# Kernel tuning notes

Hardware: AMD Instinct MI355X
Metric: run time of the kernel (lower is better)

## Reference

```python
import jax, jax.numpy as jnp
import numpy as np

M = 0.4
EPS = 1e-3
S = 64.0


def setup_inputs() -> dict:
    key = jax.random.key(0)
    k1, k2, k3, k4 = jax.random.split(key, 4)
    B, C = 1024, 100000
    # cosine logits strictly inside (-1, 1) so acos is finite
    logits = jax.random.uniform(k1, (B, C), jnp.float32, minval=-0.99, maxval=0.99)
    # feature norms around the typical face-embedding range
    norms = jax.random.uniform(k2, (B, 1), jnp.float32, minval=5.0, maxval=35.0)
    labels = jax.random.randint(k3, (B,), 0, C, dtype=jnp.int64)
    neg = jax.random.uniform(k4, (B,)) < 0.05
    labels = jnp.where(neg, jnp.int64(-1), labels)
    return {"logits": logits, "norms": norms, "labels": labels}


def reference(logits, norms, labels):
    B, C = logits.shape
    pos = labels != -1                                   # [B]
    # safe_norms is detached in the original (clone().detach())
    sn = jax.lax.stop_gradient(jnp.clip(norms, 1e-3, 100.0))[:, 0]  # [B]
    posf = pos.astype(sn.dtype)
    cnt = jnp.sum(posf)
    mean = jnp.sum(sn * posf) / cnt                      # mean over positive rows
    var = jnp.sum(jnp.where(pos, (sn - mean) ** 2, 0.0)) / (cnt - 1.0)  # unbiased, like torch.std
    std = jnp.sqrt(var)
    margin_scaler = (sn - mean) / (std + EPS)            # [B]
    g_angular = -M * margin_scaler                        # added to theta at target column
    g_add = M + M * margin_scaler                         # subtracted from cos at target column

    rows = jnp.arange(B)
    theta = jnp.arccos(logits)                           # [B, C]
    # inject angular margin only at (row, label); 0 for skipped rows (label=-1 wraps harmlessly)
    theta = theta.at[rows, labels].add(jnp.where(pos, g_angular, 0.0))
    tl = jnp.cos(jnp.clip(theta, EPS, jnp.pi - EPS))     # [B, C]
    tl = tl.at[rows, labels].add(-jnp.where(pos, g_add, 0.0))
    # rows with label == -1 keep their original logits
    out = jnp.where(pos[:, None], tl, logits) * S
    return out
```

## Files before the change

kernel.cpp:

```cpp
#include <hip/hip_runtime.h>
#include <math.h>

#define MARGIN 0.4f
#define EPSF   1e-3f
#define SCALE  64.0f
#define ELEMS_PER_THREAD 16

typedef float vfloat4 __attribute__((ext_vector_type(4)));

__global__ __launch_bounds__(256)
void adaface_scale_kernel(const vfloat4* __restrict__ in,
                          vfloat4* __restrict__ out,
                          long n4, const float* __restrict__ in_s,
                          float* __restrict__ out_s, long n_tail_start, long n) {
    long nthreads = (long)gridDim.x * blockDim.x;
    long i = (long)blockIdx.x * blockDim.x + threadIdx.x;

#pragma unroll
    for (int j = 0; j < ELEMS_PER_THREAD; ++j) {
        long k = i + (long)j * nthreads;
        if (k < n4) {
            vfloat4 v = __builtin_nontemporal_load(&in[k]);
            v *= SCALE;
            __builtin_nontemporal_store(v, &out[k]);
        }
    }
    for (long k = n_tail_start + i; k < n; k += nthreads) {
        out_s[k] = in_s[k] * SCALE;
    }
}

__global__ __launch_bounds__(1024)
void adaface_fixup_kernel(const float* __restrict__ logits,
                          const float* __restrict__ norms,
                          const int* __restrict__ labels,
                          float* __restrict__ out, int B, int C) {
    __shared__ float red_a[16];
    __shared__ float red_b[16];
    __shared__ float s_cnt, s_mean, s_std;

    int tid  = threadIdx.x;
    int lane = tid & 63;
    int wave = tid >> 6;
    int nw   = (blockDim.x + 63) >> 6;

    float sn  = 0.0f;
    int   lab = -1;
    bool  pos = false;
    if (tid < B) {
        sn  = fminf(fmaxf(norms[tid], 1e-3f), 100.0f);
        lab = labels[tid];
        pos = (lab != -1);
    }

    float a = pos ? 1.0f : 0.0f;
    float b = pos ? sn : 0.0f;
    for (int off = 32; off >= 1; off >>= 1) {
        a += __shfl_down(a, off);
        b += __shfl_down(b, off);
    }
    if (lane == 0) { red_a[wave] = a; red_b[wave] = b; }
    __syncthreads();
    if (wave == 0) {
        float aa = (lane < nw) ? red_a[lane] : 0.0f;
        float bb = (lane < nw) ? red_b[lane] : 0.0f;
        for (int off = 32; off >= 1; off >>= 1) {
            aa += __shfl_down(aa, off);
            bb += __shfl_down(bb, off);
        }
        if (lane == 0) { s_cnt = aa; s_mean = bb / aa; }
    }
    __syncthreads();

    float mean = s_mean;
    float d = sn - mean;
    float v = pos ? d * d : 0.0f;
    for (int off = 32; off >= 1; off >>= 1) v += __shfl_down(v, off);
    if (lane == 0) red_a[wave] = v;
    __syncthreads();
    if (wave == 0) {
        float vv = (lane < nw) ? red_a[lane] : 0.0f;
        for (int off = 32; off >= 1; off >>= 1) vv += __shfl_down(vv, off);
        if (lane == 0) s_std = sqrtf(vv / (s_cnt - 1.0f));
    }
    __syncthreads();

    if (tid < B && pos) {
        float ms    = (sn - mean) / (s_std + EPSF);
        float g_ang = -MARGIN * ms;
        float g_add = MARGIN + MARGIN * ms;
        long idx = (long)tid * C + lab;
        float x = logits[idx];
        float theta = acosf(x) + g_ang;
        theta = fminf(fmaxf(theta, EPSF), (float)M_PI - EPSF);
        out[idx] = (cosf(theta) - g_add) * SCALE;
    }
}

extern "C" void kernel_launch(void* const* d_in, const int* in_sizes, int n_in,
                              void* d_out, int out_size, void* d_ws, size_t ws_size,
                              hipStream_t stream) {
    const float* logits = (const float*)d_in[0];
    const float* norms  = (const float*)d_in[1];
    const int*   labels = (const int*)d_in[2];
    float* out = (float*)d_out;

    int B = in_sizes[2];
    long n = (long)in_sizes[0];
    int C = (int)(n / B);

    long n4 = n / 4;
    long tail_start = n4 * 4;

    int block = 256;
    long grid_l = (n4 + (long)block * ELEMS_PER_THREAD - 1) / ((long)block * ELEMS_PER_THREAD);
    int grid = (int)grid_l;

    adaface_scale_kernel<<<grid, block, 0, stream>>>(
        (const vfloat4*)logits, (vfloat4*)out, n4,
        logits, out, tail_start, n);

    adaface_fixup_kernel<<<1, 1024, 0, stream>>>(logits, norms, labels, out, B, C);
}
```

Baseline: 147.9 us.

## Fuse margin fixup into streaming scale kernel with per-block target patching

Merges the separate single-block fixup kernel into the main scale kernel. Each block now owns a contiguous chunk and checks whether one of its at most two overlapping rows has its target column inside that chunk. Blocks that do recompute the norm mean and std redundantly, apply the angular margin, and patch the value into the vector store. This removes a second launch and its serial tail, at the cost of redundant reductions in target-holding blocks and a fixed limit of 1024 rows for the statistics.

Result: slower. 157.6 us (+6.5%).

```diff
diff --git a/kernel.cpp b/kernel.cpp
--- a/kernel.cpp
+++ b/kernel.cpp
@@ -4,96 +4,135 @@
 #define MARGIN 0.4f
 #define EPSF   1e-3f
 #define SCALE  64.0f
-#define ELEMS_PER_THREAD 16
+#define EPT    16
+#define BLK    256
 
 typedef float vfloat4 __attribute__((ext_vector_type(4)));
 
-__global__ __launch_bounds__(256)
-void adaface_scale_kernel(const vfloat4* __restrict__ in,
-                          vfloat4* __restrict__ out,
-                          long n4, const float* __restrict__ in_s,
-                          float* __restrict__ out_s, long n_tail_start, long n) {
-    long nthreads = (long)gridDim.x * blockDim.x;
-    long i = (long)blockIdx.x * blockDim.x + threadIdx.x;
+__global__ __launch_bounds__(BLK)
+void adaface_fused_kernel(const float* __restrict__ in_s,
+                          const float* __restrict__ norms,
+                          const int* __restrict__ labels,
+                          float* __restrict__ out_s,
+                          long n4, long n, int B, int C) {
+    const vfloat4* __restrict__ in  = (const vfloat4*)in_s;
+    vfloat4* __restrict__ out = (vfloat4*)out_s;
 
+    int  tid    = threadIdx.x;
+    long f4base = (long)blockIdx.x * (BLK * EPT);
+    long fstart = f4base * 4;
+    long fend   = fstart + (long)BLK * EPT * 4;
+
+    int  row0     = (int)(fstart / C);
+    long rowsplit = (long)(row0 + 1) * C;
+    int  r1       = row0 + 1;
+
+    int  lab0 = (row0 < B) ? labels[row0] : -1;
+    int  lab1 = (r1   < B) ? labels[r1]   : -1;
+    long t0 = (lab0 != -1) ? (long)row0 * C + lab0 : (long)-1;
+    long t1 = (lab1 != -1) ? (long)r1   * C + lab1 : (long)-1;
+    bool has0 = (t0 >= fstart) && (t0 < fend);
+    bool has1 = (t1 >= fstart) && (t1 < fend);
+    bool full = (f4base + (long)BLK * EPT) <= n4;
+
+    if (full && !(has0 || has1)) {
 #pragma unroll
-    for (int j = 0; j < ELEMS_PER_THREAD; ++j) {
-        long k = i + (long)j * nthreads;
-        if (k < n4) {
+        for (int j = 0; j < EPT; ++j) {
+            long k = f4base + j * BLK + tid;
             vfloat4 v = __builtin_nontemporal_load(&in[k]);
             v *= SCALE;
             __builtin_nontemporal_store(v, &out[k]);
         }
-    }
-    for (long k = n_tail_start + i; k < n; k += nthreads) {
-        out_s[k] = in_s[k] * SCALE;
-    }
-}
+    } else {
+        float v0 = 0.0f, v1 = 0.0f;
+        if (has0 || has1) {
+            __shared__ float ra[4], rb[4];
+            __shared__ float sm[3];
 
-__global__ __launch_bounds__(1024)
-void adaface_fixup_kernel(const float* __restrict__ logits,
-                          const float* __restrict__ norms,
-                          const int* __restrict__ labels,
-                          float* __restrict__ out, int B, int C) {
-    __shared__ float red_a[16];
-    __shared__ float red_b[16];
-    __shared__ float s_cnt, s_mean, s_std;
+            float lsn[4]; bool lp[4];
+            float lsum = 0.0f, lcnt = 0.0f;
+#pragma unroll
+            for (int q = 0; q < 4; ++q) {
+                int r = tid + q * BLK;
+                bool p = false; float s = 0.0f;
+                if (r < B) {
+                    int lb = labels[r];
+                    p = (lb != -1);
+                    s = fminf(fmaxf(norms[r], 1e-3f), 100.0f);
+                }
+                lp[q] = p; lsn[q] = s;
+                if (p) { lsum += s; lcnt += 1.0f; }
+            }
+            int lane = tid & 63, wv = tid >> 6;
+            for (int off = 32; off >= 1; off >>= 1) {
+                lsum += __shfl_down(lsum, off);
+                lcnt += __shfl_down(lcnt, off);
+            }
+            if (lane == 0) { ra[wv] = lsum; rb[wv] = lcnt; }
+            __syncthreads();
+            if (tid == 0) {
+                float s = ra[0] + ra[1] + ra[2] + ra[3];
+                float c = rb[0] + rb[1] + rb[2] + rb[3];
+                sm[0] = s / c; sm[2] = c;
+            }
+            __syncthreads();
+            float mean = sm[0];
+            float lvar = 0.0f;
+#pragma unroll
+            for (int q = 0; q < 4; ++q) {
+                if (lp[q]) { float d = lsn[q] - mean; lvar += d * d; }
+            }
+            for (int off = 32; off >= 1; off >>= 1) lvar += __shfl_down(lvar, off);
+            if (lane == 0) ra[wv] = lvar;
+            __syncthreads();
+            if (tid == 0) {
+                float v = ra[0] + ra[1] + ra[2] + ra[3];
+                sm[1] = sqrtf(v / (sm[2] - 1.0f));
+            }
+            __syncthreads();
+            float stdv = sm[1];
 
-    int tid  = threadIdx.x;
-    int lane = tid & 63;
-    int wave = tid >> 6;
-    int nw   = (blockDim.x + 63) >> 6;
-
-    float sn  = 0.0f;
-    int   lab = -1;
-    bool  pos = false;
-    if (tid < B) {
-        sn  = fminf(fmaxf(norms[tid], 1e-3f), 100.0f);
-        lab = labels[tid];
-        pos = (lab != -1);
+            if (has0) {
+                float sn0 = fminf(fmaxf(norms[row0], 1e-3f), 100.0f);
+                float ms  = (sn0 - mean) / (stdv + EPSF);
+                float x   = in_s[t0];
+                float th  = acosf(x) - MARGIN * ms;
+                th = fminf(fmaxf(th, EPSF), (float)M_PI - EPSF);
+                v0 = (cosf(th) - (MARGIN + MARGIN * ms)) * SCALE;
+            }
+            if (has1) {
+                float sn1 = fminf(fmaxf(norms[r1], 1e-3f), 100.0f);
+                float ms  = (sn1 - mean) / (stdv + EPSF);
+                float x   = in_s[t1];
+                float th  = acosf(x) - MARGIN * ms;
+                th = fminf(fmaxf(th, EPSF), (float)M_PI - EPSF);
+                v1 = (cosf(th) - (MARGIN + MARGIN * ms)) * SCALE;
+            }
+        }
+#pragma unroll
+        for (int j = 0; j < EPT; ++j) {
+            long k = f4base + j * BLK + tid;
+            if (k < n4) {
+                long f = k * 4;
+                vfloat4 v = __builtin_nontemporal_load(&in[k]);
+                v *= SCALE;
+                bool  in0 = f < rowsplit;
+                long  tg  = in0 ? t0 : t1;
+                float tv  = in0 ? v0 : v1;
+                long  dl  = tg - f;
+                v.x = (dl == 0) ? tv : v.x;
+                v.y = (dl == 1) ? tv : v.y;
+                v.z = (dl == 2) ? tv : v.z;
+                v.w = (dl == 3) ? tv : v.w;
+                __builtin_nontemporal_store(v, &out[k]);
+            }
+        }
     }
 
-    float a = pos ? 1.0f : 0.0f;
-    float b = pos ? sn : 0.0f;
-    for (int off = 32; off >= 1; off >>= 1) {
-        a += __shfl_down(a, off);
-        b += __shfl_down(b, off);
-    }
-    if (lane == 0) { red_a[wave] = a; red_b[wave] = b; }
-    __syncthreads();
-    if (wave == 0) {
-        float aa = (lane < nw) ? red_a[lane] : 0.0f;
-        float bb = (lane < nw) ? red_b[lane] : 0.0f;
-        for (int off = 32; off >= 1; off >>= 1) {
-            aa += __shfl_down(aa, off);
-            bb += __shfl_down(bb, off);
-        }
-        if (lane == 0) { s_cnt = aa; s_mean = bb / aa; }
-    }
-    __syncthreads();
-
-    float mean = s_mean;
-    float d = sn - mean;
-    float v = pos ? d * d : 0.0f;
-    for (int off = 32; off >= 1; off >>= 1) v += __shfl_down(v, off);
-    if (lane == 0) red_a[wave] = v;
-    __syncthreads();
-    if (wave == 0) {
-        float vv = (lane < nw) ? red_a[lane] : 0.0f;
-        for (int off = 32; off >= 1; off >>= 1) vv += __shfl_down(vv, off);
-        if (lane == 0) s_std = sqrtf(vv / (s_cnt - 1.0f));
-    }
-    __syncthreads();
-
-    if (tid < B && pos) {
-        float ms    = (sn - mean) / (s_std + EPSF);
-        float g_ang = -MARGIN * ms;
-        float g_add = MARGIN + MARGIN * ms;
-        long idx = (long)tid * C + lab;
-        float x = logits[idx];
-        float theta = acosf(x) + g_ang;
-        theta = fminf(fmaxf(theta, EPSF), (float)M_PI - EPSF);
-        out[idx] = (cosf(theta) - g_add) * SCALE;
+    long gid = (long)blockIdx.x * BLK + tid;
+    long nth = (long)gridDim.x * BLK;
+    for (long k = n4 * 4 + gid; k < n; k += nth) {
+        out_s[k] = in_s[k] * SCALE;
     }
 }
 
@@ -105,20 +144,14 @@
     const int*   labels = (const int*)d_in[2];
     float* out = (float*)d_out;
 
-    int B = in_sizes[2];
+    int  B = in_sizes[2];
     long n = (long)in_sizes[0];
-    int C = (int)(n / B);
+    int  C = (int)(n / B);
 
     long n4 = n / 4;
-    long tail_start = n4 * 4;
+    long grid_l = (n4 + (long)BLK * EPT - 1) / ((long)BLK * EPT);
+    int  grid = (int)grid_l;
 
-    int block = 256;
-    long grid_l = (n4 + (long)block * ELEMS_PER_THREAD - 1) / ((long)block * ELEMS_PER_THREAD);
-    int grid = (int)grid_l;
-
-    adaface_scale_kernel<<<grid, block, 0, stream>>>(
-        (const vfloat4*)logits, (vfloat4*)out, n4,
-        logits, out, tail_start, n);
-
-    adaface_fixup_kernel<<<1, 1024, 0, stream>>>(logits, norms, labels, out, B, C);
+    adaface_fused_kernel<<<grid, BLK, 0, stream>>>(
+        logits, norms, labels, out, n4, n, B, C);
 }
```
